# Optimization experiments

Hardware: AMD Instinct MI355X
Metric: run time of the kernel (lower is better)

## Reference

```python
import jax, jax.numpy as jnp
import numpy as np

BATCH, IN_WIDTH, OUT_FEATURES, FAN_IN = 512, 4096, 4096, 128

def setup_inputs() -> dict:
    key = jax.random.key(0)
    k1, k2, k3, k4 = jax.random.split(key, 4)
    input = jax.random.normal(k1, (BATCH, IN_WIDTH), dtype=jnp.float32)
    weight = jax.random.normal(k2, (OUT_FEATURES, FAN_IN), dtype=jnp.float32)
    bias = jax.random.normal(k3, (OUT_FEATURES,), dtype=jnp.float32)
    indx_seqs = jax.random.randint(k4, (OUT_FEATURES, FAN_IN), 0, IN_WIDTH, dtype=jnp.int64)
    return {"input": input, "weight": weight, "bias": bias, "indx_seqs": indx_seqs}

def reference(input, weight, bias, indx_seqs):
    # gather: (B, out_features, fan_in)
    gathered = input[:, indx_seqs]
    # elementwise mul with weight (out_features, fan_in), reduce over fan_in
    return jnp.einsum('bof,of->bo', gathered, weight) + bias
```

## Files before the change

kernel.cpp:

```cpp
#include <hip/hip_runtime.h>
#include <hip/hip_bf16.h>

#define BATCH    512
#define IN_WIDTH 4096
#define OUT_F    4096
#define FAN_IN   128
#define BCHUNK   16
#define NBG      (BATCH / BCHUNK)
#define OBLK     512
#define NOG      (OUT_F / OBLK)

typedef float    v2f __attribute__((ext_vector_type(2)));
typedef uint32_t v4u __attribute__((ext_vector_type(4)));

__global__ __launch_bounds__(256) void k_transpose_in(const float* __restrict__ in,
                                                      uint16_t* __restrict__ inTg) {
  __shared__ float tile[32][33];
  const int jt = blockIdx.x * 32;
  const int bt = blockIdx.y * 32;
  const int tx = threadIdx.x;
  const int ty = threadIdx.y;
#pragma unroll
  for (int r = 0; r < 32; r += 8) {
    tile[ty + r][tx] = in[(size_t)(bt + ty + r) * IN_WIDTH + (jt + tx)];
  }
  __syncthreads();
#pragma unroll
  for (int r = 0; r < 32; r += 8) {
    const int b = bt + tx;
    const int j = jt + ty + r;
    __hip_bfloat16 hv = __float2bfloat16(tile[tx][ty + r]);
    inTg[((size_t)(b >> 4) * IN_WIDTH + j) * BCHUNK + (b & 15)] =
        *reinterpret_cast<const uint16_t*>(&hv);
  }
}

__global__ __launch_bounds__(256) void k_pack(const int* __restrict__ idx,
                                              const float* __restrict__ weight,
                                              uint2* __restrict__ pk) {
  const int i = blockIdx.x * 256 + threadIdx.x;
  uint2 e;
  e.x = (uint32_t)idx[i];
  e.y = __float_as_uint(weight[i]);
  pk[i] = e;
}

__global__ __launch_bounds__(1024, 4) void k_gather_lds(const uint16_t* __restrict__ inTg,
                                                        const uint2* __restrict__ pk,
                                                        const float* __restrict__ bias,
                                                        float* __restrict__ out) {
  extern __shared__ char lds[];
  const int og = blockIdx.x;
  const int bg = blockIdx.y;
  const int t  = threadIdx.x;

  {
    const v4u* __restrict__ src =
        reinterpret_cast<const v4u*>(inTg + (size_t)bg * IN_WIDTH * BCHUNK);
    v4u* dst = reinterpret_cast<v4u*>(lds);
#pragma unroll
    for (int i = 0; i < 8; ++i) dst[i * 1024 + t] = src[i * 1024 + t];
  }
  __syncthreads();

  const int wv = t >> 6;
  const int l  = t & 63;
  const int o  = og * OBLK + wv * 32 + (l >> 1);
  const int p  = l & 1;

  const uint32_t sb = (uint32_t)(size_t)lds + (uint32_t)(p * 16);

  const uint4* __restrict__ pko =
      reinterpret_cast<const uint4*>(pk + (size_t)o * FAN_IN);

  v2f a0 = {0.f, 0.f}, a1 = {0.f, 0.f}, a2 = {0.f, 0.f}, a3 = {0.f, 0.f};

#define DSREAD(d, jj) \
  asm volatile("ds_read_b128 %0, %1" : "=v"(d) : "v"(sb + ((jj) << 5)))

#define WAIT4() do { asm volatile("s_waitcnt lgkmcnt(4)" ::: "memory"); \
                     __builtin_amdgcn_sched_barrier(0); } while (0)
#define WAIT0() do { asm volatile("s_waitcnt lgkmcnt(0)" ::: "memory"); \
                     __builtin_amdgcn_sched_barrier(0); } while (0)

#define CONSUME(v, wbits)                                              \
  do {                                                                 \
    const float wf_ = __uint_as_float(wbits);                          \
    v2f w2_; w2_[0] = wf_; w2_[1] = wf_;                               \
    v2f x0_, x1_, x2_, x3_;                                            \
    x0_[0] = __uint_as_float((v).x << 16);                             \
    x0_[1] = __uint_as_float((v).x & 0xffff0000u);                     \
    x1_[0] = __uint_as_float((v).y << 16);                             \
    x1_[1] = __uint_as_float((v).y & 0xffff0000u);                     \
    x2_[0] = __uint_as_float((v).z << 16);                             \
    x2_[1] = __uint_as_float((v).z & 0xffff0000u);                     \
    x3_[0] = __uint_as_float((v).w << 16);                             \
    x3_[1] = __uint_as_float((v).w & 0xffff0000u);                     \
    a0 += x0_ * w2_; a1 += x1_ * w2_; a2 += x2_ * w2_; a3 += x3_ * w2_;\
  } while (0)

  uint4 q0a = pko[0], q0b = pko[1];
  uint4 q1a = pko[2], q1b = pko[3];
  uint4 q2a = pko[4], q2b = pko[5];
  uint4 q3a = pko[6], q3b = pko[7];

  v4u vA0, vA1, vA2, vA3, vB0, vB1, vB2, vB3;
  uint32_t wA0, wA1, wA2, wA3, wB0, wB1, wB2, wB3;

  DSREAD(vA0, q0a.x); DSREAD(vA1, q0a.z); DSREAD(vA2, q0b.x); DSREAD(vA3, q0b.z);
  wA0 = q0a.y; wA1 = q0a.w; wA2 = q0b.y; wA3 = q0b.w;

#define STEP(Cc, QI0, QI1, QR0, QR1,                                   \
             VC0, VC1, VC2, VC3, WC0, WC1, WC2, WC3,                   \
             VI0, VI1, VI2, VI3, WI0, WI1, WI2, WI3)                   \
  do {                                                                 \
    DSREAD(VI0, QI0.x); DSREAD(VI1, QI0.z);                            \
    DSREAD(VI2, QI1.x); DSREAD(VI3, QI1.z);                            \
    WI0 = QI0.y; WI1 = QI0.w; WI2 = QI1.y; WI3 = QI1.w;                \
    {                                                                  \
      const int gn_ = ((Cc) + 4 > 31) ? 31 : ((Cc) + 4);               \
      QR0 = pko[2 * gn_];                                              \
      QR1 = pko[2 * gn_ + 1];                                          \
    }                                                                  \
    WAIT4();                                                           \
    CONSUME(VC0, WC0); CONSUME(VC1, WC1);                              \
    CONSUME(VC2, WC2); CONSUME(VC3, WC3);                              \
  } while (0)

#define STEP_A(Cc, QI0, QI1, QR0, QR1)  \
  STEP(Cc, QI0, QI1, QR0, QR1,                                           \
       vA0, vA1, vA2, vA3, wA0, wA1, wA2, wA3,                           \
       vB0, vB1, vB2, vB3, wB0, wB1, wB2, wB3)
#define STEP_B(Cc, QI0, QI1, QR0, QR1)   \
  STEP(Cc, QI0, QI1, QR0, QR1,                                           \
       vB0, vB1, vB2, vB3, wB0, wB1, wB2, wB3,                           \
       vA0, vA1, vA2, vA3, wA0, wA1, wA2, wA3)

#pragma unroll 1
  for (int cb = 0; cb < 28; cb += 4) {
    STEP_A(cb + 0, q1a, q1b, q0a, q0b);
    STEP_B(cb + 1, q2a, q2b, q1a, q1b);
    STEP_A(cb + 2, q3a, q3b, q2a, q2b);
    STEP_B(cb + 3, q0a, q0b, q3a, q3b);
  }
  STEP_A(28, q1a, q1b, q0a, q0b);
  STEP_B(29, q2a, q2b, q1a, q1b);
  STEP_A(30, q3a, q3b, q2a, q2b);
  WAIT0();
  CONSUME(vB0, wB0); CONSUME(vB1, wB1); CONSUME(vB2, wB2); CONSUME(vB3, wB3);

  const float bz = bias[o];
  const float r[8] = {a0[0], a0[1], a1[0], a1[1], a2[0], a2[1], a3[0], a3[1]};
  const size_t obase = (size_t)(bg * BCHUNK + p * 8) * OUT_F + o;
#pragma unroll
  for (int i = 0; i < 8; ++i) out[obase + (size_t)i * OUT_F] = r[i] + bz;

#undef STEP_B
#undef STEP_A
#undef STEP
#undef CONSUME
#undef WAIT4
#undef WAIT0
#undef DSREAD
}

extern "C" void kernel_launch(void* const* d_in, const int* in_sizes, int n_in,
                              void* d_out, int out_size, void* d_ws, size_t ws_size,
                              hipStream_t stream) {
  const float* input  = (const float*)d_in[0];
  const float* weight = (const float*)d_in[1];
  const float* bias   = (const float*)d_in[2];
  const int*   idx    = (const int*)d_in[3];
  float* out = (float*)d_out;

  uint16_t* inTg = (uint16_t*)d_ws;
  uint2*    pk   = (uint2*)((char*)d_ws + 4u * 1024 * 1024);

  dim3 tblk(32, 8);
  k_transpose_in<<<dim3(IN_WIDTH / 32, BATCH / 32), tblk, 0, stream>>>(input, inTg);
  k_pack<<<dim3(OUT_F * FAN_IN / 256), dim3(256), 0, stream>>>(idx, weight, pk);
  k_gather_lds<<<dim3(NOG, NBG), dim3(1024), IN_WIDTH * BCHUNK * 2, stream>>>(
      inTg, pk, bias, out);
}
```

Measured before the change: 37.79 us.

## Fuse prep kernels into one launch and stage LDS via direct global-to-LDS loads

The input-transpose and index/weight pack kernels are merged into a single launch that picks its role from the block index. This removes one kernel launch and the serialization gap between the two prep kernels. The gather kernel now fills its LDS tile with 16-byte global_load_lds instructions instead of loading through registers and then writing to LDS, which saves VGPRs and instructions. This relies on gfx950 support for 16-byte direct-to-LDS loads and on the per-wave LDS address layout matching the old one.

```diff
diff --git a/kernel.cpp b/kernel.cpp
--- a/kernel.cpp
+++ b/kernel.cpp
@@ -13,36 +13,39 @@
 typedef float    v2f __attribute__((ext_vector_type(2)));
 typedef uint32_t v4u __attribute__((ext_vector_type(4)));
 
-__global__ __launch_bounds__(256) void k_transpose_in(const float* __restrict__ in,
-                                                      uint16_t* __restrict__ inTg) {
+__global__ __launch_bounds__(256) void k_prep(const float* __restrict__ in,
+                                              const int* __restrict__ idx,
+                                              const float* __restrict__ weight,
+                                              uint16_t* __restrict__ inTg,
+                                              uint2* __restrict__ pk) {
   __shared__ float tile[32][33];
-  const int jt = blockIdx.x * 32;
-  const int bt = blockIdx.y * 32;
-  const int tx = threadIdx.x;
-  const int ty = threadIdx.y;
+  const int blk = blockIdx.x;
+  const int t   = threadIdx.x;
+  if (blk < 2048) {
+    const int jt = (blk & 127) * 32;
+    const int bt = (blk >> 7) * 32;
+    const int tx = t & 31;
+    const int ty = t >> 5;
 #pragma unroll
-  for (int r = 0; r < 32; r += 8) {
-    tile[ty + r][tx] = in[(size_t)(bt + ty + r) * IN_WIDTH + (jt + tx)];
+    for (int r = 0; r < 32; r += 8) {
+      tile[ty + r][tx] = in[(size_t)(bt + ty + r) * IN_WIDTH + (jt + tx)];
+    }
+    __syncthreads();
+#pragma unroll
+    for (int r = 0; r < 32; r += 8) {
+      const int b = bt + tx;
+      const int j = jt + ty + r;
+      __hip_bfloat16 hv = __float2bfloat16(tile[tx][ty + r]);
+      inTg[((size_t)(b >> 4) * IN_WIDTH + j) * BCHUNK + (b & 15)] =
+          *reinterpret_cast<const uint16_t*>(&hv);
+    }
+  } else {
+    const int i = (blk - 2048) * 256 + t;
+    uint2 e;
+    e.x = (uint32_t)idx[i];
+    e.y = __float_as_uint(weight[i]);
+    pk[i] = e;
   }
-  __syncthreads();
-#pragma unroll
-  for (int r = 0; r < 32; r += 8) {
-    const int b = bt + tx;
-    const int j = jt + ty + r;
-    __hip_bfloat16 hv = __float2bfloat16(tile[tx][ty + r]);
-    inTg[((size_t)(b >> 4) * IN_WIDTH + j) * BCHUNK + (b & 15)] =
-        *reinterpret_cast<const uint16_t*>(&hv);
-  }
-}
-
-__global__ __launch_bounds__(256) void k_pack(const int* __restrict__ idx,
-                                              const float* __restrict__ weight,
-                                              uint2* __restrict__ pk) {
-  const int i = blockIdx.x * 256 + threadIdx.x;
-  uint2 e;
-  e.x = (uint32_t)idx[i];
-  e.y = __float_as_uint(weight[i]);
-  pk[i] = e;
 }
 
 __global__ __launch_bounds__(1024, 4) void k_gather_lds(const uint16_t* __restrict__ inTg,
@@ -57,9 +60,15 @@
   {
     const v4u* __restrict__ src =
         reinterpret_cast<const v4u*>(inTg + (size_t)bg * IN_WIDTH * BCHUNK);
-    v4u* dst = reinterpret_cast<v4u*>(lds);
 #pragma unroll
-    for (int i = 0; i < 8; ++i) dst[i * 1024 + t] = src[i * 1024 + t];
+    for (int i = 0; i < 8; ++i) {
+      const v4u* g = src + i * 1024 + t;
+      char* d = lds + ((t >> 6) << 10) + (i << 14);
+      __builtin_amdgcn_global_load_lds(
+          (const __attribute__((address_space(1))) void*)g,
+          (__attribute__((address_space(3))) void*)d, 16, 0, 0);
+    }
+    asm volatile("s_waitcnt vmcnt(0)" ::: "memory");
   }
   __syncthreads();
 
@@ -88,14 +97,14 @@
     const float wf_ = __uint_as_float(wbits);                          \
     v2f w2_; w2_[0] = wf_; w2_[1] = wf_;                               \
     v2f x0_, x1_, x2_, x3_;                                            \
-    x0_[0] = __uint_as_float((v).x << 16);                             \
-    x0_[1] = __uint_as_float((v).x & 0xffff0000u);                     \
-    x1_[0] = __uint_as_float((v).y << 16);                             \
-    x1_[1] = __uint_as_float((v).y & 0xffff0000u);                     \
-    x2_[0] = __uint_as_float((v).z << 16);                             \
-    x2_[1] = __uint_as_float((v).z & 0xffff0000u);                     \
-    x3_[0] = __uint_as_float((v).w << 16);                             \
-    x3_[1] = __uint_as_float((v).w & 0xffff0000u);                     \
+    x0_[0] = __uint_as_float((v)[0] << 16);                            \
+    x0_[1] = __uint_as_float((v)[0] & 0xffff0000u);                    \
+    x1_[0] = __uint_as_float((v)[1] << 16);                            \
+    x1_[1] = __uint_as_float((v)[1] & 0xffff0000u);                    \
+    x2_[0] = __uint_as_float((v)[2] << 16);                            \
+    x2_[1] = __uint_as_float((v)[2] & 0xffff0000u);                    \
+    x3_[0] = __uint_as_float((v)[3] << 16);                            \
+    x3_[1] = __uint_as_float((v)[3] & 0xffff0000u);                    \
     a0 += x0_ * w2_; a1 += x1_ * w2_; a2 += x2_ * w2_; a3 += x3_ * w2_;\
   } while (0)
 
@@ -127,11 +136,11 @@
     CONSUME(VC2, WC2); CONSUME(VC3, WC3);                              \
   } while (0)
 
-#define STEP_A(Cc, QI0, QI1, QR0, QR1)  \
+#define STEP_A(Cc, QI0, QI1, QR0, QR1)                                   \
   STEP(Cc, QI0, QI1, QR0, QR1,                                           \
        vA0, vA1, vA2, vA3, wA0, wA1, wA2, wA3,                           \
        vB0, vB1, vB2, vB3, wB0, wB1, wB2, wB3)
-#define STEP_B(Cc, QI0, QI1, QR0, QR1)   \
+#define STEP_B(Cc, QI0, QI1, QR0, QR1)                                   \
   STEP(Cc, QI0, QI1, QR0, QR1,                                           \
        vB0, vB1, vB2, vB3, wB0, wB1, wB2, wB3,                           \
        vA0, vA1, vA2, vA3, wA0, wA1, wA2, wA3)
@@ -176,9 +185,7 @@
   uint16_t* inTg = (uint16_t*)d_ws;
   uint2*    pk   = (uint2*)((char*)d_ws + 4u * 1024 * 1024);
 
-  dim3 tblk(32, 8);
-  k_transpose_in<<<dim3(IN_WIDTH / 32, BATCH / 32), tblk, 0, stream>>>(input, inTg);
-  k_pack<<<dim3(OUT_F * FAN_IN / 256), dim3(256), 0, stream>>>(idx, weight, pk);
+  k_prep<<<dim3(4096), dim3(256), 0, stream>>>(input, idx, weight, inTg, pk);
   k_gather_lds<<<dim3(NOG, NBG), dim3(1024), IN_WIDTH * BCHUNK * 2, stream>>>(
       inTg, pk, bias, out);
 }
```

Measured after the change: 35.89 us. 1.05x faster.
